# Kernel optimization log

Measured on AMD Instinct MI355X. Metric: run time of the kernel, lower is better.

The kernel has to match this reference:

```python
import jax, jax.numpy as jnp
import numpy as np

T = 1024
V = 512
K_BINS = jnp.array([1, 2, 3, 4, 5, 6, 7, 8, 12, 16, 24, 32, 48, 64, 96, 128], dtype=jnp.int32)
SPLIT_T = T // 2                      # int(T * 0.5)
CW = max(4, T // 20)                  # crossfade width = 51
FADE_START = SPLIT_T - CW // 2        # 487
FADE_END = SPLIT_T + CW // 2          # 537


def _early_weight():
    t = jnp.arange(T, dtype=jnp.float32)
    fade = 1.0 - (t - FADE_START) / (FADE_END - FADE_START)
    ew = jnp.where(t < FADE_START, 1.0, jnp.where(t < FADE_END, fade, 0.0))
    return ew.reshape(1, T, 1)


def setup_inputs() -> dict:
    key = jax.random.key(0)
    k = jax.random.split(key, 5)
    B = 64
    return {
        "x": jax.random.normal(k[0], (B, T, V), dtype=jnp.float32),
        "g_early_real": jax.random.normal(k[1], (V, 16), dtype=jnp.float32) * 0.1,
        "g_early_imag": jax.random.normal(k[2], (V, 16), dtype=jnp.float32) * 0.1,
        "g_late_real": jax.random.normal(k[3], (V, 16), dtype=jnp.float32) * 0.1,
        "g_late_imag": jax.random.normal(k[4], (V, 16), dtype=jnp.float32) * 0.1,
    }


def reference(x, g_early_real, g_early_imag, g_late_real, g_late_imag):
    # x: [B, T, V] real. rfft along time.
    X = jnp.fft.rfft(x, n=T, axis=1)              # [B, F, V] complex, F = T//2+1
    xb = X[:, K_BINS, :]                          # [B, K, V]
    # complex gain (1 + gr + i*gi), broadcast [1, K, V]
    g_e = (g_early_real + 1j * g_early_imag).T[None, :, :]
    g_l = (g_late_real + 1j * g_late_imag).T[None, :, :]
    Y_e = X.at[:, K_BINS, :].set(xb * (1.0 + g_e))
    Y_l = X.at[:, K_BINS, :].set(xb * (1.0 + g_l))
    y_early = jnp.fft.irfft(Y_e, n=T, axis=1)     # [B, T, V]
    y_late = jnp.fft.irfft(Y_l, n=T, axis=1)
    ew = _early_weight()
    return ew * y_early + (1.0 - ew) * y_late
```

## Files before the change

### kernel.cpp

```cpp
#include <hip/hip_runtime.h>
#include <math.h>

#define T_LEN 1024
#define VV 512
#define BB 64
#define NB 16
#define ANG_STEP 0.006135923151542565f
#define FADE_S 487
#define FADE_E 537
#define ATL 64

typedef float v4f __attribute__((ext_vector_type(4)));

__device__ constexpr int KB[NB] = {1,2,3,4,5,6,7,8,12,16,24,32,48,64,96,128};

template<int TLEN>
__global__ __launch_bounds__(256, 2) void k_dft_partial(const float* __restrict__ x,
                                                        float* __restrict__ xpart,
                                                        int tcx_count) {
    const int b    = blockIdx.x;
    const int tc   = blockIdx.y;
    const int tid  = threadIdx.x;
    const int h    = tid >> 7;
    const int lane = tid & 127;
    const int t0   = tc * TLEN;
    const int HT   = TLEN / 2;

    __shared__ float2 tab[TLEN][NB];
    for (int i = tid; i < TLEN * NB; i += 256) {
        int t = i >> 4, j = i & 15;
        int idx = (KB[j] * (t0 + t)) & (T_LEN - 1);
        float ss, cc; sincosf(ANG_STEP * (float)idx, &ss, &cc);
        tab[t][j] = make_float2(cc, ss);
    }
    __syncthreads();

    float xr0[NB], xi0[NB], xr1[NB], xi1[NB];
    float xr2[NB], xi2[NB], xr3[NB], xi3[NB];
#pragma unroll
    for (int j = 0; j < NB; ++j) {
        xr0[j] = xi0[j] = xr1[j] = xi1[j] = 0.0f;
        xr2[j] = xi2[j] = xr3[j] = xi3[j] = 0.0f;
    }

    const int th0 = h * HT;
    const float4* xrd = (const float4*)(x + ((size_t)b * T_LEN + t0 + th0) * VV) + lane;

#define DFT_T(TT, AV)                                           \
    do {                                                        \
        _Pragma("unroll")                                       \
        for (int j = 0; j < NB; ++j) {                          \
            float2 cs = tab[th0 + (TT)][j];                     \
            xr0[j] = fmaf((AV).x, cs.x, xr0[j]);                \
            xi0[j] = fmaf(-(AV).x, cs.y, xi0[j]);               \
            xr1[j] = fmaf((AV).y, cs.x, xr1[j]);                \
            xi1[j] = fmaf(-(AV).y, cs.y, xi1[j]);               \
            xr2[j] = fmaf((AV).z, cs.x, xr2[j]);                \
            xi2[j] = fmaf(-(AV).z, cs.y, xi2[j]);               \
            xr3[j] = fmaf((AV).w, cs.x, xr3[j]);                \
            xi3[j] = fmaf(-(AV).w, cs.y, xi3[j]);               \
        }                                                       \
    } while (0)

    float4 a0 = xrd[(size_t)0 * 128];
    float4 a1 = xrd[(size_t)1 * 128];
    float4 a2 = xrd[(size_t)2 * 128];
    float4 a3 = xrd[(size_t)3 * 128];
#pragma unroll 1
    for (int t = 0; t < HT - 4; t += 4) {
        float4 b0 = xrd[(size_t)(t + 4) * 128];
        float4 b1 = xrd[(size_t)(t + 5) * 128];
        float4 b2 = xrd[(size_t)(t + 6) * 128];
        float4 b3 = xrd[(size_t)(t + 7) * 128];
        DFT_T(t + 0, a0); DFT_T(t + 1, a1); DFT_T(t + 2, a2); DFT_T(t + 3, a3);
        a0 = b0; a1 = b1; a2 = b2; a3 = b3;
    }
    {
        const int t = HT - 4;
        DFT_T(t + 0, a0); DFT_T(t + 1, a1); DFT_T(t + 2, a2); DFT_T(t + 3, a3);
    }
#undef DFT_T

    const int tcx = tc * 2 + h;
    float4* o = (float4*)(xpart + (size_t)(b * tcx_count + tcx) * 32 * VV) + lane;
#pragma unroll
    for (int j = 0; j < NB; ++j) {
        o[(size_t)j        * 128] = make_float4(xr0[j], xr1[j], xr2[j], xr3[j]);
        o[(size_t)(NB + j) * 128] = make_float4(xi0[j], xi1[j], xi2[j], xi3[j]);
    }
}

__global__ __launch_bounds__(256) void k_combine(const float* __restrict__ xpart,
                                                 const float* __restrict__ ger,
                                                 const float* __restrict__ gei,
                                                 const float* __restrict__ glr,
                                                 const float* __restrict__ gli,
                                                 float* __restrict__ H, int tc_count) {
    const int b   = blockIdx.x;
    const int j   = blockIdx.y;
    const int tid = threadIdx.x;
    const int v0  = tid * 2;

    float re0 = 0.f, re1 = 0.f, im0 = 0.f, im1 = 0.f;
#pragma unroll 8
    for (int tc = 0; tc < tc_count; ++tc) {
        const float2* p = (const float2*)(xpart + (size_t)(b * tc_count + tc) * 32 * VV) + tid;
        float2 a  = p[(size_t)j        * 256];
        float2 bb = p[(size_t)(NB + j) * 256];
        re0 += a.x;  re1 += a.y;
        im0 += bb.x; im1 += bb.y;
    }

    const float scale = 2.0f / (float)T_LEN;
    float er0 = ger[v0 * NB + j],       ei0 = gei[v0 * NB + j];
    float lr0 = glr[v0 * NB + j],       li0 = gli[v0 * NB + j];
    float er1 = ger[(v0 + 1) * NB + j], ei1 = gei[(v0 + 1) * NB + j];
    float lr1 = glr[(v0 + 1) * NB + j], li1 = gli[(v0 + 1) * NB + j];

    float here0 = (re0 * er0 - im0 * ei0) * scale;
    float heim0 = (re0 * ei0 + im0 * er0) * scale;
    float hlre0 = (re0 * lr0 - im0 * li0) * scale;
    float hlim0 = (re0 * li0 + im0 * lr0) * scale;
    float here1 = (re1 * er1 - im1 * ei1) * scale;
    float heim1 = (re1 * ei1 + im1 * er1) * scale;
    float hlre1 = (re1 * lr1 - im1 * li1) * scale;
    float hlim1 = (re1 * li1 + im1 * lr1) * scale;

    float2* o = (float2*)(H + (size_t)b * 64 * VV) + tid;
    o[(size_t)j        * 256] = make_float2(here0, here1);
    o[(size_t)(16 + j) * 256] = make_float2(-heim0, -heim1);
    o[(size_t)(32 + j) * 256] = make_float2(hlre0, hlre1);
    o[(size_t)(48 + j) * 256] = make_float2(-hlim0, -hlim1);
}

__global__ __launch_bounds__(128, 2) void k_apply(const float* __restrict__ x,
                                                  const float* __restrict__ H,
                                                  float* __restrict__ out) {
    const int b    = blockIdx.x;
    const int tile = blockIdx.y;
    const int tid  = threadIdx.x;
    const int t0   = tile * ATL;
    const int qo   = (tile < 8) ? 0 : 32;

    __shared__ float2 tab[ATL][NB];
    for (int i = tid; i < ATL * NB; i += 128) {
        int t = i >> 4, j = i & 15;
        int idx = (KB[j] * (t0 + t)) & (T_LEN - 1);
        float ss, cc; sincosf(ANG_STEP * (float)idx, &ss, &cc);
        tab[t][j] = make_float2(cc, ss);
    }

    float hr0[NB], hi0[NB], hr1[NB], hi1[NB];
    float hr2[NB], hi2[NB], hr3[NB], hi3[NB];
    const float4* hp = (const float4*)(H + (size_t)b * 64 * VV) + tid;
#pragma unroll
    for (int j = 0; j < NB; ++j) {
        float4 a  = hp[(size_t)(qo + j)      * 128];
        hr0[j] = a.x;  hr1[j] = a.y;  hr2[j] = a.z;  hr3[j] = a.w;
        float4 bq = hp[(size_t)(qo + 16 + j) * 128];
        hi0[j] = bq.x; hi1[j] = bq.y; hi2[j] = bq.z; hi3[j] = bq.w;
    }
    __syncthreads();

    const float4* xrd = (const float4*)(x + ((size_t)b * T_LEN + t0) * VV) + tid;
    v4f*          ow  = (v4f*)(out + ((size_t)b * T_LEN + t0) * VV) + tid;

#define APPLY_T(TT, AV)                                         \
    do {                                                        \
        float s0 = 0.f, s1 = 0.f, s2 = 0.f, s3 = 0.f;           \
        _Pragma("unroll")                                       \
        for (int j = 0; j < NB; ++j) {                          \
            float2 cs = tab[(TT)][j];                           \
            s0 = fmaf(hr0[j], cs.x, s0);                        \
            s0 = fmaf(hi0[j], cs.y, s0);                        \
            s1 = fmaf(hr1[j], cs.x, s1);                        \
            s1 = fmaf(hi1[j], cs.y, s1);                        \
            s2 = fmaf(hr2[j], cs.x, s2);                        \
            s2 = fmaf(hi2[j], cs.y, s2);                        \
            s3 = fmaf(hr3[j], cs.x, s3);                        \
            s3 = fmaf(hi3[j], cs.y, s3);                        \
        }                                                       \
        v4f ov; ov.x = (AV).x + s0; ov.y = (AV).y + s1;         \
        ov.z = (AV).z + s2; ov.w = (AV).w + s3;                 \
        __builtin_nontemporal_store(ov,                         \
            &ow[(size_t)(TT) * 128]);                           \
    } while (0)

    float4 a0 = xrd[(size_t)0 * 128];
    float4 a1 = xrd[(size_t)1 * 128];
    float4 a2 = xrd[(size_t)2 * 128];
    float4 a3 = xrd[(size_t)3 * 128];
#pragma unroll 1
    for (int t = 0; t < ATL - 4; t += 4) {
        float4 b0 = xrd[(size_t)(t + 4) * 128];
        float4 b1 = xrd[(size_t)(t + 5) * 128];
        float4 b2 = xrd[(size_t)(t + 6) * 128];
        float4 b3 = xrd[(size_t)(t + 7) * 128];
        APPLY_T(t + 0, a0); APPLY_T(t + 1, a1); APPLY_T(t + 2, a2); APPLY_T(t + 3, a3);
        a0 = b0; a1 = b1; a2 = b2; a3 = b3;
    }
    {
        const int t = ATL - 4;
        APPLY_T(t + 0, a0); APPLY_T(t + 1, a1); APPLY_T(t + 2, a2); APPLY_T(t + 3, a3);
    }
#undef APPLY_T
}

__global__ __launch_bounds__(512) void k_fixup(const float* __restrict__ x,
                                               const float* __restrict__ H,
                                               float* __restrict__ out) {
    const int b   = blockIdx.x;
    const int tz  = blockIdx.y;
    const int tid = threadIdx.x;
    const int ts  = tz ? 512 : FADE_S;
    const int te  = tz ? FADE_E : 512;
    const int nt  = te - ts;

    __shared__ float2 tab[32][NB];
    for (int i = tid; i < nt * NB; i += 512) {
        int t = i >> 4, j = i & 15;
        int idx = (KB[j] * (ts + t)) & (T_LEN - 1);
        float ss, cc; sincosf(ANG_STEP * (float)idx, &ss, &cc);
        tab[t][j] = make_float2(cc, ss);
    }

    float er[NB], ei[NB], lr[NB], li[NB];
    const float* hp = H + (size_t)b * 64 * VV + tid;
#pragma unroll
    for (int j = 0; j < NB; ++j) {
        er[j] = hp[(size_t)j        * VV];
        ei[j] = hp[(size_t)(16 + j) * VV];
        lr[j] = hp[(size_t)(32 + j) * VV];
        li[j] = hp[(size_t)(48 + j) * VV];
    }
    __syncthreads();

    const float* xrd = x + ((size_t)b * T_LEN + ts) * VV + tid;
    float*       ow  = out + ((size_t)b * T_LEN + ts) * VV + tid;

    for (int t = 0; t < nt; ++t) {
        float av = xrd[(size_t)t * VV];
        const int tg = ts + t;
        float se = 0.f, sl = 0.f;
#pragma unroll
        for (int j = 0; j < NB; ++j) {
            float2 cs = tab[t][j];
            se = fmaf(er[j], cs.x, se); se = fmaf(ei[j], cs.y, se);
            sl = fmaf(lr[j], cs.x, sl); sl = fmaf(li[j], cs.y, sl);
        }
        float w = 1.0f - (float)(tg - FADE_S) * (1.0f / 50.0f);
        ow[(size_t)t * VV] = av + fmaf(w, se - sl, sl);
    }
}

extern "C" void kernel_launch(void* const* d_in, const int* in_sizes, int n_in,
                              void* d_out, int out_size, void* d_ws, size_t ws_size,
                              hipStream_t stream) {
    (void)in_sizes; (void)n_in; (void)out_size;
    const float* x   = (const float*)d_in[0];
    const float* ger = (const float*)d_in[1];
    const float* gei = (const float*)d_in[2];
    const float* glr = (const float*)d_in[3];
    const float* gli = (const float*)d_in[4];
    float* out = (float*)d_out;

    const size_t hflts = (size_t)BB * 64 * VV;
    int tcx;
    if (((size_t)BB * 16 * 32 * VV + hflts) * sizeof(float) <= ws_size) tcx = 16;
    else                                                                tcx = 8;

    float* xpart = (float*)d_ws;
    float* H     = xpart + (size_t)BB * tcx * 32 * VV;

    if (tcx == 16) k_dft_partial<128><<<dim3(BB, 8), 256, 0, stream>>>(x, xpart, 16);
    else           k_dft_partial<256><<<dim3(BB, 4), 256, 0, stream>>>(x, xpart, 8);

    k_combine<<<dim3(BB, NB), 256, 0, stream>>>(xpart, ger, gei, glr, gli, H, tcx);
    k_apply<<<dim3(BB, 16), 128, 0, stream>>>(x, H, out);
    k_fixup<<<dim3(BB, 2), 512, 0, stream>>>(x, H, out);
}
```

Baseline: 114.9 us.

## Fuse DFT, gain combine and apply into one kernel per batch-column chunk

Result: slower. 119.9 us (+4.3%).

```diff
diff --git a/kernel.cpp b/kernel.cpp
--- a/kernel.cpp
+++ b/kernel.cpp
@@ -8,200 +8,186 @@
 #define ANG_STEP 0.006135923151542565f
 #define FADE_S 487
 #define FADE_E 537
-#define ATL 64
 
 typedef float v4f __attribute__((ext_vector_type(4)));
 
 __device__ constexpr int KB[NB] = {1,2,3,4,5,6,7,8,12,16,24,32,48,64,96,128};
-
-template<int TLEN>
-__global__ __launch_bounds__(256, 2) void k_dft_partial(const float* __restrict__ x,
-                                                        float* __restrict__ xpart,
-                                                        int tcx_count) {
-    const int b    = blockIdx.x;
-    const int tc   = blockIdx.y;
-    const int tid  = threadIdx.x;
-    const int h    = tid >> 7;
-    const int lane = tid & 127;
-    const int t0   = tc * TLEN;
-    const int HT   = TLEN / 2;
-
-    __shared__ float2 tab[TLEN][NB];
-    for (int i = tid; i < TLEN * NB; i += 256) {
+__device__ constexpr float SGN[NB] = {-1.f, 1.f, -1.f, 1.f, -1.f, 1.f, -1.f, 1.f,
+                                       1.f, 1.f,  1.f, 1.f,  1.f, 1.f,  1.f, 1.f};
+
+__global__ __launch_bounds__(512, 1) void k_fused(const float* __restrict__ x,
+                                                  const float* __restrict__ ger,
+                                                  const float* __restrict__ gei,
+                                                  const float* __restrict__ glr,
+                                                  const float* __restrict__ gli,
+                                                  float* __restrict__ Hg,
+                                                  float* __restrict__ out) {
+    const int b   = blockIdx.x;
+    const int vc  = blockIdx.y;
+    const int tid = threadIdx.x;
+    const int vt  = tid & 31;
+    const int th  = tid >> 5;
+
+    __shared__ __align__(16) float2 tab[512][NB];
+    __shared__ __align__(16) float  HB[64 * 128];
+    float* scr = (float*)tab;
+
+    for (int i = tid; i < 512 * NB; i += 512) {
         int t = i >> 4, j = i & 15;
-        int idx = (KB[j] * (t0 + t)) & (T_LEN - 1);
+        int idx = (KB[j] * t) & (T_LEN - 1);
         float ss, cc; sincosf(ANG_STEP * (float)idx, &ss, &cc);
         tab[t][j] = make_float2(cc, ss);
     }
     __syncthreads();
 
-    float xr0[NB], xi0[NB], xr1[NB], xi1[NB];
-    float xr2[NB], xi2[NB], xr3[NB], xi3[NB];
-#pragma unroll
-    for (int j = 0; j < NB; ++j) {
-        xr0[j] = xi0[j] = xr1[j] = xi1[j] = 0.0f;
-        xr2[j] = xi2[j] = xr3[j] = xi3[j] = 0.0f;
-    }
-
-    const int th0 = h * HT;
-    const float4* xrd = (const float4*)(x + ((size_t)b * T_LEN + t0 + th0) * VV) + lane;
+    float ar[4][NB], ai[4][NB];
+#pragma unroll
+    for (int k = 0; k < 4; ++k)
+#pragma unroll
+        for (int j = 0; j < NB; ++j) { ar[k][j] = 0.f; ai[k][j] = 0.f; }
+
+    const int tbase = th * 64;
+    const int ttab  = tbase & 511;
+    const float4* xrd = (const float4*)(x + ((size_t)b * T_LEN + tbase) * VV + vc * 128) + vt;
 
 #define DFT_T(TT, AV)                                           \
     do {                                                        \
         _Pragma("unroll")                                       \
         for (int j = 0; j < NB; ++j) {                          \
-            float2 cs = tab[th0 + (TT)][j];                     \
-            xr0[j] = fmaf((AV).x, cs.x, xr0[j]);                \
-            xi0[j] = fmaf(-(AV).x, cs.y, xi0[j]);               \
-            xr1[j] = fmaf((AV).y, cs.x, xr1[j]);                \
-            xi1[j] = fmaf(-(AV).y, cs.y, xi1[j]);               \
-            xr2[j] = fmaf((AV).z, cs.x, xr2[j]);                \
-            xi2[j] = fmaf(-(AV).z, cs.y, xi2[j]);               \
-            xr3[j] = fmaf((AV).w, cs.x, xr3[j]);                \
-            xi3[j] = fmaf(-(AV).w, cs.y, xi3[j]);               \
+            float2 cs = tab[ttab + (TT)][j];                    \
+            ar[0][j] = fmaf((AV).x, cs.x, ar[0][j]);            \
+            ai[0][j] = fmaf(-(AV).x, cs.y, ai[0][j]);           \
+            ar[1][j] = fmaf((AV).y, cs.x, ar[1][j]);            \
+            ai[1][j] = fmaf(-(AV).y, cs.y, ai[1][j]);           \
+            ar[2][j] = fmaf((AV).z, cs.x, ar[2][j]);            \
+            ai[2][j] = fmaf(-(AV).z, cs.y, ai[2][j]);           \
+            ar[3][j] = fmaf((AV).w, cs.x, ar[3][j]);            \
+            ai[3][j] = fmaf(-(AV).w, cs.y, ai[3][j]);           \
         }                                                       \
     } while (0)
 
-    float4 a0 = xrd[(size_t)0 * 128];
-    float4 a1 = xrd[(size_t)1 * 128];
-    float4 a2 = xrd[(size_t)2 * 128];
-    float4 a3 = xrd[(size_t)3 * 128];
+    {
+        float4 a0 = xrd[(size_t)0 * 128];
+        float4 a1 = xrd[(size_t)1 * 128];
+        float4 a2 = xrd[(size_t)2 * 128];
+        float4 a3 = xrd[(size_t)3 * 128];
 #pragma unroll 1
-    for (int t = 0; t < HT - 4; t += 4) {
-        float4 b0 = xrd[(size_t)(t + 4) * 128];
-        float4 b1 = xrd[(size_t)(t + 5) * 128];
-        float4 b2 = xrd[(size_t)(t + 6) * 128];
-        float4 b3 = xrd[(size_t)(t + 7) * 128];
-        DFT_T(t + 0, a0); DFT_T(t + 1, a1); DFT_T(t + 2, a2); DFT_T(t + 3, a3);
-        a0 = b0; a1 = b1; a2 = b2; a3 = b3;
-    }
-    {
-        const int t = HT - 4;
-        DFT_T(t + 0, a0); DFT_T(t + 1, a1); DFT_T(t + 2, a2); DFT_T(t + 3, a3);
+        for (int i = 0; i < 60; i += 4) {
+            float4 b0 = xrd[(size_t)(i + 4) * 128];
+            float4 b1 = xrd[(size_t)(i + 5) * 128];
+            float4 b2 = xrd[(size_t)(i + 6) * 128];
+            float4 b3 = xrd[(size_t)(i + 7) * 128];
+            DFT_T(i + 0, a0); DFT_T(i + 1, a1); DFT_T(i + 2, a2); DFT_T(i + 3, a3);
+            a0 = b0; a1 = b1; a2 = b2; a3 = b3;
+        }
+        DFT_T(60, a0); DFT_T(61, a1); DFT_T(62, a2); DFT_T(63, a3);
     }
 #undef DFT_T
 
-    const int tcx = tc * 2 + h;
-    float4* o = (float4*)(xpart + (size_t)(b * tcx_count + tcx) * 32 * VV) + lane;
-#pragma unroll
-    for (int j = 0; j < NB; ++j) {
-        o[(size_t)j        * 128] = make_float4(xr0[j], xr1[j], xr2[j], xr3[j]);
-        o[(size_t)(NB + j) * 128] = make_float4(xi0[j], xi1[j], xi2[j], xi3[j]);
-    }
-}
-
-__global__ __launch_bounds__(256) void k_combine(const float* __restrict__ xpart,
-                                                 const float* __restrict__ ger,
-                                                 const float* __restrict__ gei,
-                                                 const float* __restrict__ glr,
-                                                 const float* __restrict__ gli,
-                                                 float* __restrict__ H, int tc_count) {
-    const int b   = blockIdx.x;
-    const int j   = blockIdx.y;
-    const int tid = threadIdx.x;
-    const int v0  = tid * 2;
-
-    float re0 = 0.f, re1 = 0.f, im0 = 0.f, im1 = 0.f;
-#pragma unroll 8
-    for (int tc = 0; tc < tc_count; ++tc) {
-        const float2* p = (const float2*)(xpart + (size_t)(b * tc_count + tc) * 32 * VV) + tid;
-        float2 a  = p[(size_t)j        * 256];
-        float2 bb = p[(size_t)(NB + j) * 256];
-        re0 += a.x;  re1 += a.y;
-        im0 += bb.x; im1 += bb.y;
-    }
+    if (th >= 8) {
+#pragma unroll
+        for (int k = 0; k < 4; ++k)
+#pragma unroll
+            for (int j = 0; j < NB; ++j) { ar[k][j] *= SGN[j]; ai[k][j] *= SGN[j]; }
+    }
+
+    __syncthreads();
 
     const float scale = 2.0f / (float)T_LEN;
-    float er0 = ger[v0 * NB + j],       ei0 = gei[v0 * NB + j];
-    float lr0 = glr[v0 * NB + j],       li0 = gli[v0 * NB + j];
-    float er1 = ger[(v0 + 1) * NB + j], ei1 = gei[(v0 + 1) * NB + j];
-    float lr1 = glr[(v0 + 1) * NB + j], li1 = gli[(v0 + 1) * NB + j];
-
-    float here0 = (re0 * er0 - im0 * ei0) * scale;
-    float heim0 = (re0 * ei0 + im0 * er0) * scale;
-    float hlre0 = (re0 * lr0 - im0 * li0) * scale;
-    float hlim0 = (re0 * li0 + im0 * lr0) * scale;
-    float here1 = (re1 * er1 - im1 * ei1) * scale;
-    float heim1 = (re1 * ei1 + im1 * er1) * scale;
-    float hlre1 = (re1 * lr1 - im1 * li1) * scale;
-    float hlim1 = (re1 * li1 + im1 * lr1) * scale;
-
-    float2* o = (float2*)(H + (size_t)b * 64 * VV) + tid;
-    o[(size_t)j        * 256] = make_float2(here0, here1);
-    o[(size_t)(16 + j) * 256] = make_float2(-heim0, -heim1);
-    o[(size_t)(32 + j) * 256] = make_float2(hlre0, hlre1);
-    o[(size_t)(48 + j) * 256] = make_float2(-hlim0, -hlim1);
-}
-
-__global__ __launch_bounds__(128, 2) void k_apply(const float* __restrict__ x,
-                                                  const float* __restrict__ H,
-                                                  float* __restrict__ out) {
-    const int b    = blockIdx.x;
-    const int tile = blockIdx.y;
-    const int tid  = threadIdx.x;
-    const int t0   = tile * ATL;
-    const int qo   = (tile < 8) ? 0 : 32;
-
-    __shared__ float2 tab[ATL][NB];
-    for (int i = tid; i < ATL * NB; i += 128) {
+#pragma unroll
+    for (int r = 0; r < 4; ++r) {
+        const int j0 = r * 4;
+#pragma unroll
+        for (int k = 0; k < 4; ++k) {
+            const int v = vt * 4 + k;
+            float4* w = (float4*)(scr + (size_t)(th * 128 + v) * 8);
+            w[0] = make_float4(ar[k][j0 + 0], ar[k][j0 + 1], ar[k][j0 + 2], ar[k][j0 + 3]);
+            w[1] = make_float4(ai[k][j0 + 0], ai[k][j0 + 1], ai[k][j0 + 2], ai[k][j0 + 3]);
+        }
+        __syncthreads();
+        {
+            const int v  = tid & 127;
+            const int jj = tid >> 7;
+            const int j  = j0 + jj;
+            float Xre = 0.f, Xim = 0.f;
+#pragma unroll
+            for (int t2 = 0; t2 < 16; ++t2) {
+                Xre += scr[(size_t)(t2 * 128 + v) * 8 + jj];
+                Xim += scr[(size_t)(t2 * 128 + v) * 8 + 4 + jj];
+            }
+            const int vg = vc * 128 + v;
+            float er = ger[vg * NB + j], ei = gei[vg * NB + j];
+            float lr = glr[vg * NB + j], li = gli[vg * NB + j];
+            float here  = (Xre * er - Xim * ei) * scale;
+            float heimN = -(Xre * ei + Xim * er) * scale;
+            float hlre  = (Xre * lr - Xim * li) * scale;
+            float hlimN = -(Xre * li + Xim * lr) * scale;
+            HB[j * 128 + v]        = here;
+            HB[(16 + j) * 128 + v] = heimN;
+            HB[(32 + j) * 128 + v] = hlre;
+            HB[(48 + j) * 128 + v] = hlimN;
+            float* hg = Hg + (size_t)b * 64 * VV + vg;
+            hg[(size_t)j * VV]        = here;
+            hg[(size_t)(16 + j) * VV] = heimN;
+            hg[(size_t)(32 + j) * VV] = hlre;
+            hg[(size_t)(48 + j) * VV] = hlimN;
+        }
+        __syncthreads();
+    }
+
+    for (int i = tid; i < 512 * NB; i += 512) {
         int t = i >> 4, j = i & 15;
-        int idx = (KB[j] * (t0 + t)) & (T_LEN - 1);
+        int idx = (KB[j] * t) & (T_LEN - 1);
         float ss, cc; sincosf(ANG_STEP * (float)idx, &ss, &cc);
         tab[t][j] = make_float2(cc, ss);
     }
-
-    float hr0[NB], hi0[NB], hr1[NB], hi1[NB];
-    float hr2[NB], hi2[NB], hr3[NB], hi3[NB];
-    const float4* hp = (const float4*)(H + (size_t)b * 64 * VV) + tid;
+    __syncthreads();
+
+    float hr0[NB], hr1[NB], hr2[NB], hr3[NB];
+    float hi0[NB], hi1[NB], hi2[NB], hi3[NB];
+    const int qb = (th < 8) ? 0 : 32;
 #pragma unroll
     for (int j = 0; j < NB; ++j) {
-        float4 a  = hp[(size_t)(qo + j)      * 128];
-        hr0[j] = a.x;  hr1[j] = a.y;  hr2[j] = a.z;  hr3[j] = a.w;
-        float4 bq = hp[(size_t)(qo + 16 + j) * 128];
-        hi0[j] = bq.x; hi1[j] = bq.y; hi2[j] = bq.z; hi3[j] = bq.w;
-    }
-    __syncthreads();
-
-    const float4* xrd = (const float4*)(x + ((size_t)b * T_LEN + t0) * VV) + tid;
-    v4f*          ow  = (v4f*)(out + ((size_t)b * T_LEN + t0) * VV) + tid;
-
-#define APPLY_T(TT, AV)                                         \
-    do {                                                        \
-        float s0 = 0.f, s1 = 0.f, s2 = 0.f, s3 = 0.f;           \
-        _Pragma("unroll")                                       \
-        for (int j = 0; j < NB; ++j) {                          \
-            float2 cs = tab[(TT)][j];                           \
-            s0 = fmaf(hr0[j], cs.x, s0);                        \
-            s0 = fmaf(hi0[j], cs.y, s0);                        \
-            s1 = fmaf(hr1[j], cs.x, s1);                        \
-            s1 = fmaf(hi1[j], cs.y, s1);                        \
-            s2 = fmaf(hr2[j], cs.x, s2);                        \
-            s2 = fmaf(hi2[j], cs.y, s2);                        \
-            s3 = fmaf(hr3[j], cs.x, s3);                        \
-            s3 = fmaf(hi3[j], cs.y, s3);                        \
-        }                                                       \
-        v4f ov; ov.x = (AV).x + s0; ov.y = (AV).y + s1;         \
-        ov.z = (AV).z + s2; ov.w = (AV).w + s3;                 \
-        __builtin_nontemporal_store(ov,                         \
-            &ow[(size_t)(TT) * 128]);                           \
+        const float4 a  = *(const float4*)&HB[(qb + j)      * 128 + vt * 4];
+        const float4 bq = *(const float4*)&HB[(qb + 16 + j) * 128 + vt * 4];
+        const float sg = (th >= 8) ? SGN[j] : 1.0f;
+        hr0[j] = a.x * sg;  hr1[j] = a.y * sg;  hr2[j] = a.z * sg;  hr3[j] = a.w * sg;
+        hi0[j] = bq.x * sg; hi1[j] = bq.y * sg; hi2[j] = bq.z * sg; hi3[j] = bq.w * sg;
+    }
+
+    v4f* ow = (v4f*)(out + ((size_t)b * T_LEN + tbase) * VV + vc * 128) + vt;
+
+#define APPLY_T(TT, AV)                                               \
+    do {                                                              \
+        float s0 = 0.f, s1 = 0.f, s2 = 0.f, s3 = 0.f;                 \
+        _Pragma("unroll")                                             \
+        for (int j = 0; j < NB; ++j) {                                \
+            float2 cs = tab[ttab + (TT)][j];                          \
+            s0 = fmaf(hr0[j], cs.x, s0); s0 = fmaf(hi0[j], cs.y, s0); \
+            s1 = fmaf(hr1[j], cs.x, s1); s1 = fmaf(hi1[j], cs.y, s1); \
+            s2 = fmaf(hr2[j], cs.x, s2); s2 = fmaf(hi2[j], cs.y, s2); \
+            s3 = fmaf(hr3[j], cs.x, s3); s3 = fmaf(hi3[j], cs.y, s3); \
+        }                                                             \
+        v4f ov; ov.x = (AV).x + s0; ov.y = (AV).y + s1;               \
+        ov.z = (AV).z + s2; ov.w = (AV).w + s3;                       \
+        __builtin_nontemporal_store(ov, &ow[(size_t)(TT) * 128]);     \
     } while (0)
 
-    float4 a0 = xrd[(size_t)0 * 128];
-    float4 a1 = xrd[(size_t)1 * 128];
-    float4 a2 = xrd[(size_t)2 * 128];
-    float4 a3 = xrd[(size_t)3 * 128];
+    {
+        float4 a0 = xrd[(size_t)0 * 128];
+        float4 a1 = xrd[(size_t)1 * 128];
+        float4 a2 = xrd[(size_t)2 * 128];
+        float4 a3 = xrd[(size_t)3 * 128];
 #pragma unroll 1
-    for (int t = 0; t < ATL - 4; t += 4) {
-        float4 b0 = xrd[(size_t)(t + 4) * 128];
-        float4 b1 = xrd[(size_t)(t + 5) * 128];
-        float4 b2 = xrd[(size_t)(t + 6) * 128];
-        float4 b3 = xrd[(size_t)(t + 7) * 128];
-        APPLY_T(t + 0, a0); APPLY_T(t + 1, a1); APPLY_T(t + 2, a2); APPLY_T(t + 3, a3);
-        a0 = b0; a1 = b1; a2 = b2; a3 = b3;
-    }
-    {
-        const int t = ATL - 4;
-        APPLY_T(t + 0, a0); APPLY_T(t + 1, a1); APPLY_T(t + 2, a2); APPLY_T(t + 3, a3);
+        for (int i = 0; i < 60; i += 4) {
+            float4 b0 = xrd[(size_t)(i + 4) * 128];
+            float4 b1 = xrd[(size_t)(i + 5) * 128];
+            float4 b2 = xrd[(size_t)(i + 6) * 128];
+            float4 b3 = xrd[(size_t)(i + 7) * 128];
+            APPLY_T(i + 0, a0); APPLY_T(i + 1, a1); APPLY_T(i + 2, a2); APPLY_T(i + 3, a3);
+            a0 = b0; a1 = b1; a2 = b2; a3 = b3;
+        }
+        APPLY_T(60, a0); APPLY_T(61, a1); APPLY_T(62, a2); APPLY_T(63, a3);
     }
 #undef APPLY_T
 }
@@ -256,7 +242,7 @@
 extern "C" void kernel_launch(void* const* d_in, const int* in_sizes, int n_in,
                               void* d_out, int out_size, void* d_ws, size_t ws_size,
                               hipStream_t stream) {
-    (void)in_sizes; (void)n_in; (void)out_size;
+    (void)in_sizes; (void)n_in; (void)out_size; (void)ws_size;
     const float* x   = (const float*)d_in[0];
     const float* ger = (const float*)d_in[1];
     const float* gei = (const float*)d_in[2];
@@ -264,18 +250,8 @@
     const float* gli = (const float*)d_in[4];
     float* out = (float*)d_out;
 
-    const size_t hflts = (size_t)BB * 64 * VV;
-    int tcx;
-    if (((size_t)BB * 16 * 32 * VV + hflts) * sizeof(float) <= ws_size) tcx = 16;
-    else                                                                tcx = 8;
-
-    float* xpart = (float*)d_ws;
-    float* H     = xpart + (size_t)BB * tcx * 32 * VV;
-
-    if (tcx == 16) k_dft_partial<128><<<dim3(BB, 8), 256, 0, stream>>>(x, xpart, 16);
-    else           k_dft_partial<256><<<dim3(BB, 4), 256, 0, stream>>>(x, xpart, 8);
-
-    k_combine<<<dim3(BB, NB), 256, 0, stream>>>(xpart, ger, gei, glr, gli, H, tcx);
-    k_apply<<<dim3(BB, 16), 128, 0, stream>>>(x, H, out);
-    k_fixup<<<dim3(BB, 2), 512, 0, stream>>>(x, H, out);
+    float* Hg = (float*)d_ws;
+
+    k_fused<<<dim3(BB, 4), 512, 0, stream>>>(x, ger, gei, glr, gli, Hg, out);
+    k_fixup<<<dim3(BB, 2), 512, 0, stream>>>(x, Hg, out);
 }
```
